# Optimization experiments

Measured on AMD Instinct MI355X. Metric: run time of the kernel, lower is better.

Reference implementation:

```python
import jax, jax.numpy as jnp
import numpy as np

B, OUT, IN = 1024, 1024, 512


def setup_inputs() -> dict:
    key = jax.random.key(0)
    kx, kw = jax.random.split(key)
    X = jax.random.normal(kx, (B, IN), dtype=jnp.float32)
    # Xavier-uniform init for W [out_features, in_features]
    limit = float(np.sqrt(6.0 / (IN + OUT)))
    W = jax.random.uniform(kw, (OUT, IN), dtype=jnp.float32, minval=-limit, maxval=limit)
    return {"X": X, "W": W}


def reference(X, W):
    # tropical min-plus + max-plus 'matmul':
    # out[b,o] = min_i(W[o,i] + X[b,i]) + max_i(W[o,i] + X[b,i])
    S = X[:, None, :] + W[None, :, :]  # [B, OUT, IN]
    return jnp.min(S, axis=-1) + jnp.max(S, axis=-1)  # [B, OUT]
```

## Files before the change

kernel.cpp:

```cpp
#include <hip/hip_runtime.h>
#include <math.h>


typedef float f4 __attribute__((ext_vector_type(4)));

constexpr int B_DIM  = 1024;
constexpr int O_DIM  = 1024;
constexpr int IN_DIM = 512;

constexpr int TM     = 64;
constexpr int TN     = 32;
constexpr int KW     = 128;
constexpr int BK     = 8;
constexpr int NSTAGE = KW / BK;

__global__ __launch_bounds__(256) void tropical_gemm(
    const float* __restrict__ X, const float* __restrict__ W,
    float* __restrict__ out) {
    __shared__ float lds[8192];

    const int tid  = threadIdx.x;
    const int w    = tid >> 6;
    const int lane = tid & 63;
    const int im   = lane >> 3;
    const int in_  = lane & 7;
    const int b0   = blockIdx.y * TM;
    const int o0   = blockIdx.x * TN;
    const int xoff = im * 8;
    const int woff = in_ * 4;
    const int wrow = lane >> 1;
    const int wk4  = (lane & 1) * 4;

    const float* Xp = X + (size_t)(b0 + lane) * IN_DIM + w * KW;
    const float* Wp = W + (size_t)(o0 + wrow) * IN_DIM + w * KW + wk4;

    float* wbase = &lds[w * 1536];

    float mn[8][4], mx[8][4];
#pragma unroll
    for (int i = 0; i < 8; ++i)
#pragma unroll
        for (int j = 0; j < 4; ++j) { mn[i][j] = INFINITY; mx[i][j] = -INFINITY; }

#define STAGE(bufsel)                                                         \
    do {                                                                      \
        float* d_ = wbase + (bufsel) * 768;                                   \
        _Pragma("unroll")                                                     \
        for (int j_ = 0; j_ < 4; ++j_) {                                      \
            d_[j_ * 64 + lane]       = xa[j_];                                \
            d_[(4 + j_) * 64 + lane] = xb[j_];                                \
            d_[512 + (wk4 + j_) * 32 + wrow] = wv[j_];                        \
        }                                                                     \
    } while (0)

#define LOADQ(P, kp)                                                          \
    do {                                                                      \
        P##x0  = *(const f4*)(sXf + (2 * (kp)) * 64 + xoff);                  \
        P##x0b = *(const f4*)(sXf + (2 * (kp)) * 64 + xoff + 4);              \
        P##x1  = *(const f4*)(sXf + (2 * (kp) + 1) * 64 + xoff);              \
        P##x1b = *(const f4*)(sXf + (2 * (kp) + 1) * 64 + xoff + 4);          \
        P##w0  = *(const f4*)(sWf + (2 * (kp)) * 32 + woff);                  \
        P##w1  = *(const f4*)(sWf + (2 * (kp) + 1) * 32 + woff);              \
    } while (0)

#define COMPUTE(P)                                                            \
    do {                                                                      \
        _Pragma("unroll")                                                     \
        for (int a_ = 0; a_ < 8; ++a_) {                                      \
            const float x0_ = (a_ < 4) ? P##x0[a_] : P##x0b[a_ - 4];          \
            const float x1_ = (a_ < 4) ? P##x1[a_] : P##x1b[a_ - 4];          \
            _Pragma("unroll")                                                 \
            for (int b_ = 0; b_ < 4; ++b_) {                                  \
                float s0_ = x0_ + P##w0[b_];                                  \
                float s1_ = x1_ + P##w1[b_];                                  \
                asm("v_min3_f32 %0, %1, %2, %0"                               \
                    : "+v"(mn[a_][b_]) : "v"(s0_), "v"(s1_));                 \
                asm("v_max3_f32 %0, %1, %2, %0"                               \
                    : "+v"(mx[a_][b_]) : "v"(s0_), "v"(s1_));                 \
            }                                                                 \
        }                                                                     \
    } while (0)

    f4 xa = *(const f4*)(Xp);
    f4 xb = *(const f4*)(Xp + 4);
    f4 wv = *(const f4*)(Wp);
    STAGE(0);

#pragma unroll 1
    for (int s = 0; s < NSTAGE; ++s) {
        if (s + 1 < NSTAGE) {
            xa = *(const f4*)(Xp + (s + 1) * BK);
            xb = *(const f4*)(Xp + (s + 1) * BK + 4);
            wv = *(const f4*)(Wp + (s + 1) * BK);
        }

        const float* sXf = wbase + (s & 1) * 768;
        const float* sWf = sXf + 512;

        f4 Ax0, Ax0b, Ax1, Ax1b, Aw0, Aw1;
        f4 Bx0, Bx0b, Bx1, Bx1b, Bw0, Bw1;

        LOADQ(A, 0);
        LOADQ(B, 1);
        COMPUTE(A);
        LOADQ(A, 2);
        COMPUTE(B);
        LOADQ(B, 3);
        COMPUTE(A);
        COMPUTE(B);

        if (s + 1 < NSTAGE) STAGE((s + 1) & 1);
    }
#undef STAGE
#undef LOADQ
#undef COMPUTE

#define DUMP_STATE(slotbase)                                                  \
    do {                                                                      \
        float* p_ = (slotbase) + lane * 4;                                    \
        _Pragma("unroll")                                                     \
        for (int r_ = 0; r_ < 8; ++r_) {                                      \
            *(float4*)(p_ + r_ * 256) =                                       \
                make_float4(mn[r_][0], mn[r_][1], mn[r_][2], mn[r_][3]);      \
            *(float4*)(p_ + (8 + r_) * 256) =                                 \
                make_float4(mx[r_][0], mx[r_][1], mx[r_][2], mx[r_][3]);      \
        }                                                                     \
    } while (0)

#define MERGE_STATE(slotbase)                                                 \
    do {                                                                      \
        const float* p_ = (slotbase) + lane * 4;                              \
        _Pragma("unroll")                                                     \
        for (int r_ = 0; r_ < 8; ++r_) {                                      \
            float4 vn_ = *(const float4*)(p_ + r_ * 256);                     \
            float4 vx_ = *(const float4*)(p_ + (8 + r_) * 256);               \
            mn[r_][0] = fminf(mn[r_][0], vn_.x);                              \
            mn[r_][1] = fminf(mn[r_][1], vn_.y);                              \
            mn[r_][2] = fminf(mn[r_][2], vn_.z);                              \
            mn[r_][3] = fminf(mn[r_][3], vn_.w);                              \
            mx[r_][0] = fmaxf(mx[r_][0], vx_.x);                              \
            mx[r_][1] = fmaxf(mx[r_][1], vx_.y);                              \
            mx[r_][2] = fmaxf(mx[r_][2], vx_.z);                              \
            mx[r_][3] = fmaxf(mx[r_][3], vx_.w);                              \
        }                                                                     \
    } while (0)

    float* slotA = lds;
    float* slotB = lds + 4096;

    __syncthreads();
    if (w == 2) DUMP_STATE(slotA);
    if (w == 3) DUMP_STATE(slotB);
    __syncthreads();
    if (w == 0) MERGE_STATE(slotA);
    if (w == 1) MERGE_STATE(slotB);
    __syncthreads();
    if (w == 1) DUMP_STATE(slotA);
    __syncthreads();
    if (w == 0) {
        MERGE_STATE(slotA);
        float* op = out + (size_t)(b0 + im * 8) * O_DIM + o0 + in_ * 4;
#pragma unroll
        for (int r = 0; r < 8; ++r)
            *(float4*)(op + (size_t)r * O_DIM) =
                make_float4(mn[r][0] + mx[r][0], mn[r][1] + mx[r][1],
                            mn[r][2] + mx[r][2], mn[r][3] + mx[r][3]);
    }
#undef DUMP_STATE
#undef MERGE_STATE
}

extern "C" void kernel_launch(void* const* d_in, const int* in_sizes, int n_in,
                              void* d_out, int out_size, void* d_ws, size_t ws_size,
                              hipStream_t stream) {
    (void)in_sizes; (void)n_in; (void)d_ws; (void)ws_size; (void)out_size;
    const float* X = (const float*)d_in[0];
    const float* W = (const float*)d_in[1];
    float* out     = (float*)d_out;

    dim3 grid(O_DIM / TN, B_DIM / TM);
    tropical_gemm<<<grid, dim3(256), 0, stream>>>(X, W, out);
}
```

Measured before the change: 31.66 us.

## Split K across eight waves per block with a deeper LDS reduction tree

Each block now runs 512 threads, and each of the eight waves handles a 64-wide K slice instead of four waves handling 128-wide slices. The per-wave pipeline gets half as many stages, and the final min/max merge becomes a three-level tree over four LDS slots. The software-pipelined A/B register double-buffering of LDS reads is replaced by a plain unrolled loop, leaving scheduling to the compiler. The aim is more parallel waves per tile to hide latency, at the cost of extra barriers and reduction traffic and doubled LDS per block.

Measured after the change: 33.74 us. 1.07x slower.

```diff
diff --git a/kernel.cpp b/kernel.cpp
--- a/kernel.cpp
+++ b/kernel.cpp
@@ -10,14 +10,14 @@
 
 constexpr int TM     = 64;
 constexpr int TN     = 32;
-constexpr int KW     = 128;
+constexpr int KW     = 64;
 constexpr int BK     = 8;
 constexpr int NSTAGE = KW / BK;
 
-__global__ __launch_bounds__(256) void tropical_gemm(
+__global__ __launch_bounds__(512, 4) void tropical_gemm(
     const float* __restrict__ X, const float* __restrict__ W,
     float* __restrict__ out) {
-    __shared__ float lds[8192];
+    __shared__ float lds[16384];
 
     const int tid  = threadIdx.x;
     const int w    = tid >> 6;
@@ -53,34 +53,6 @@
         }                                                                     \
     } while (0)
 
-#define LOADQ(P, kp)                                                          \
-    do {                                                                      \
-        P##x0  = *(const f4*)(sXf + (2 * (kp)) * 64 + xoff);                  \
-        P##x0b = *(const f4*)(sXf + (2 * (kp)) * 64 + xoff + 4);              \
-        P##x1  = *(const f4*)(sXf + (2 * (kp) + 1) * 64 + xoff);              \
-        P##x1b = *(const f4*)(sXf + (2 * (kp) + 1) * 64 + xoff + 4);          \
-        P##w0  = *(const f4*)(sWf + (2 * (kp)) * 32 + woff);                  \
-        P##w1  = *(const f4*)(sWf + (2 * (kp) + 1) * 32 + woff);              \
-    } while (0)
-
-#define COMPUTE(P)                                                            \
-    do {                                                                      \
-        _Pragma("unroll")                                                     \
-        for (int a_ = 0; a_ < 8; ++a_) {                                      \
-            const float x0_ = (a_ < 4) ? P##x0[a_] : P##x0b[a_ - 4];          \
-            const float x1_ = (a_ < 4) ? P##x1[a_] : P##x1b[a_ - 4];          \
-            _Pragma("unroll")                                                 \
-            for (int b_ = 0; b_ < 4; ++b_) {                                  \
-                float s0_ = x0_ + P##w0[b_];                                  \
-                float s1_ = x1_ + P##w1[b_];                                  \
-                asm("v_min3_f32 %0, %1, %2, %0"                               \
-                    : "+v"(mn[a_][b_]) : "v"(s0_), "v"(s1_));                 \
-                asm("v_max3_f32 %0, %1, %2, %0"                               \
-                    : "+v"(mx[a_][b_]) : "v"(s0_), "v"(s1_));                 \
-            }                                                                 \
-        }                                                                     \
-    } while (0)
-
     f4 xa = *(const f4*)(Xp);
     f4 xb = *(const f4*)(Xp + 4);
     f4 wv = *(const f4*)(Wp);
@@ -97,23 +69,33 @@
         const float* sXf = wbase + (s & 1) * 768;
         const float* sWf = sXf + 512;
 
-        f4 Ax0, Ax0b, Ax1, Ax1b, Aw0, Aw1;
-        f4 Bx0, Bx0b, Bx1, Bx1b, Bw0, Bw1;
-
-        LOADQ(A, 0);
-        LOADQ(B, 1);
-        COMPUTE(A);
-        LOADQ(A, 2);
-        COMPUTE(B);
-        LOADQ(B, 3);
-        COMPUTE(A);
-        COMPUTE(B);
+#pragma unroll
+        for (int kp = 0; kp < 4; ++kp) {
+            f4 x0  = *(const f4*)(sXf + (2 * kp) * 64 + xoff);
+            f4 x0b = *(const f4*)(sXf + (2 * kp) * 64 + xoff + 4);
+            f4 x1  = *(const f4*)(sXf + (2 * kp + 1) * 64 + xoff);
+            f4 x1b = *(const f4*)(sXf + (2 * kp + 1) * 64 + xoff + 4);
+            f4 w0  = *(const f4*)(sWf + (2 * kp) * 32 + woff);
+            f4 w1  = *(const f4*)(sWf + (2 * kp + 1) * 32 + woff);
+#pragma unroll
+            for (int a = 0; a < 8; ++a) {
+                const float xv0 = (a < 4) ? x0[a] : x0b[a - 4];
+                const float xv1 = (a < 4) ? x1[a] : x1b[a - 4];
+#pragma unroll
+                for (int b = 0; b < 4; ++b) {
+                    float s0 = xv0 + w0[b];
+                    float s1 = xv1 + w1[b];
+                    asm("v_min3_f32 %0, %1, %2, %0"
+                        : "+v"(mn[a][b]) : "v"(s0), "v"(s1));
+                    asm("v_max3_f32 %0, %1, %2, %0"
+                        : "+v"(mx[a][b]) : "v"(s0), "v"(s1));
+                }
+            }
+        }
 
         if (s + 1 < NSTAGE) STAGE((s + 1) & 1);
     }
 #undef STAGE
-#undef LOADQ
-#undef COMPUTE
 
 #define DUMP_STATE(slotbase)                                                  \
     do {                                                                      \
@@ -145,20 +127,32 @@
         }                                                                     \
     } while (0)
 
-    float* slotA = lds;
-    float* slotB = lds + 4096;
+    float* const slot0 = lds;
+    float* const slot1 = lds + 4096;
+    float* const slot2 = lds + 8192;
+    float* const slot3 = lds + 12288;
 
     __syncthreads();
-    if (w == 2) DUMP_STATE(slotA);
-    if (w == 3) DUMP_STATE(slotB);
+    if (w == 4) DUMP_STATE(slot0);
+    if (w == 5) DUMP_STATE(slot1);
+    if (w == 6) DUMP_STATE(slot2);
+    if (w == 7) DUMP_STATE(slot3);
     __syncthreads();
-    if (w == 0) MERGE_STATE(slotA);
-    if (w == 1) MERGE_STATE(slotB);
+    if (w == 0) MERGE_STATE(slot0);
+    if (w == 1) MERGE_STATE(slot1);
+    if (w == 2) MERGE_STATE(slot2);
+    if (w == 3) MERGE_STATE(slot3);
     __syncthreads();
-    if (w == 1) DUMP_STATE(slotA);
+    if (w == 2) DUMP_STATE(slot0);
+    if (w == 3) DUMP_STATE(slot1);
+    __syncthreads();
+    if (w == 0) MERGE_STATE(slot0);
+    if (w == 1) MERGE_STATE(slot1);
+    __syncthreads();
+    if (w == 1) DUMP_STATE(slot0);
     __syncthreads();
     if (w == 0) {
-        MERGE_STATE(slotA);
+        MERGE_STATE(slot0);
         float* op = out + (size_t)(b0 + im * 8) * O_DIM + o0 + in_ * 4;
 #pragma unroll
         for (int r = 0; r < 8; ++r)
@@ -179,5 +173,5 @@
     float* out     = (float*)d_out;
 
     dim3 grid(O_DIM / TN, B_DIM / TM);
-    tropical_gemm<<<grid, dim3(256), 0, stream>>>(X, W, out);
+    tropical_gemm<<<grid, dim3(512), 0, stream>>>(X, W, out);
 }
```

## Software-pipeline LDS reads and global prefetch across double-buffered stages

Applied to the files above, without the earlier changes.

Restructures the main loop to process two stages per iteration with four register fragment sets, so LDS reads for the next k-slice and the next stage are issued ahead of the min/max compute. Global prefetch now runs two stages ahead in two register sets. This is meant to hide LDS and global latency behind the v_min3/v_max3 compute. In exchange it uses more VGPRs, which may lower occupancy. It also relies on per-wave ordering of LDS writes and reads, since the wave writes a buffer it may still be reading from, with no barrier between.

Result: faster. 31.02 us (-2.0%).

```diff
diff --git a/kernel.cpp b/kernel.cpp
--- a/kernel.cpp
+++ b/kernel.cpp
@@ -42,25 +42,32 @@
 #pragma unroll
         for (int j = 0; j < 4; ++j) { mn[i][j] = INFINITY; mx[i][j] = -INFINITY; }
 
-#define STAGE(bufsel)                                                         \
+#define STAGE(bufsel, G)                                                      \
     do {                                                                      \
         float* d_ = wbase + (bufsel) * 768;                                   \
         _Pragma("unroll")                                                     \
         for (int j_ = 0; j_ < 4; ++j_) {                                      \
-            d_[j_ * 64 + lane]       = xa[j_];                                \
-            d_[(4 + j_) * 64 + lane] = xb[j_];                                \
-            d_[512 + (wk4 + j_) * 32 + wrow] = wv[j_];                        \
+            d_[j_ * 64 + lane]       = xa##G[j_];                             \
+            d_[(4 + j_) * 64 + lane] = xb##G[j_];                             \
+            d_[512 + (wk4 + j_) * 32 + wrow] = wv##G[j_];                     \
         }                                                                     \
     } while (0)
 
-#define LOADQ(P, kp)                                                          \
+#define PREFETCH(G, stg)                                                      \
     do {                                                                      \
-        P##x0  = *(const f4*)(sXf + (2 * (kp)) * 64 + xoff);                  \
-        P##x0b = *(const f4*)(sXf + (2 * (kp)) * 64 + xoff + 4);              \
-        P##x1  = *(const f4*)(sXf + (2 * (kp) + 1) * 64 + xoff);              \
-        P##x1b = *(const f4*)(sXf + (2 * (kp) + 1) * 64 + xoff + 4);          \
-        P##w0  = *(const f4*)(sWf + (2 * (kp)) * 32 + woff);                  \
-        P##w1  = *(const f4*)(sWf + (2 * (kp) + 1) * 32 + woff);              \
+        xa##G = *(const f4*)(Xp + (stg) * BK);                                \
+        xb##G = *(const f4*)(Xp + (stg) * BK + 4);                            \
+        wv##G = *(const f4*)(Wp + (stg) * BK);                                \
+    } while (0)
+
+#define LOADQ(P, cX, cW, kp)                                                  \
+    do {                                                                      \
+        P##x0  = *(const f4*)((cX) + (2 * (kp)) * 64 + xoff);                 \
+        P##x0b = *(const f4*)((cX) + (2 * (kp)) * 64 + xoff + 4);             \
+        P##x1  = *(const f4*)((cX) + (2 * (kp) + 1) * 64 + xoff);             \
+        P##x1b = *(const f4*)((cX) + (2 * (kp) + 1) * 64 + xoff + 4);         \
+        P##w0  = *(const f4*)((cW) + (2 * (kp)) * 32 + woff);                 \
+        P##w1  = *(const f4*)((cW) + (2 * (kp) + 1) * 32 + woff);             \
     } while (0)
 
 #define COMPUTE(P)                                                            \
@@ -81,37 +88,45 @@
         }                                                                     \
     } while (0)
 
-    f4 xa = *(const f4*)(Xp);
-    f4 xb = *(const f4*)(Xp + 4);
-    f4 wv = *(const f4*)(Wp);
-    STAGE(0);
+    f4 Ax0, Ax0b, Ax1, Ax1b, Aw0, Aw1;
+    f4 Bx0, Bx0b, Bx1, Bx1b, Bw0, Bw1;
+    f4 Cx0, Cx0b, Cx1, Cx1b, Cw0, Cw1;
+    f4 Dx0, Dx0b, Dx1, Dx1b, Dw0, Dw1;
+    f4 xa0, xb0, wv0, xa1, xb1, wv1;
+
+    const float* bX0 = wbase;
+    const float* bW0 = bX0 + 512;
+    const float* bX1 = wbase + 768;
+    const float* bW1 = bX1 + 512;
+
+    PREFETCH(0, 0);
+    STAGE(0, 0);
+    PREFETCH(1, 1);
+    LOADQ(A, bX0, bW0, 0);
+    LOADQ(B, bX0, bW0, 1);
 
 #pragma unroll 1
-    for (int s = 0; s < NSTAGE; ++s) {
-        if (s + 1 < NSTAGE) {
-            xa = *(const f4*)(Xp + (s + 1) * BK);
-            xb = *(const f4*)(Xp + (s + 1) * BK + 4);
-            wv = *(const f4*)(Wp + (s + 1) * BK);
+    for (int s2 = 0; s2 < 8; ++s2) {
+        LOADQ(C, bX0, bW0, 2);  COMPUTE(A);
+        LOADQ(D, bX0, bW0, 3);  COMPUTE(B);
+        STAGE(1, 1);
+        if (s2 < 7) PREFETCH(0, 2 * s2 + 2);
+        LOADQ(A, bX1, bW1, 0);  COMPUTE(C);
+        LOADQ(B, bX1, bW1, 1);  COMPUTE(D);
+
+        LOADQ(C, bX1, bW1, 2);  COMPUTE(A);
+        LOADQ(D, bX1, bW1, 3);  COMPUTE(B);
+        if (s2 < 7) {
+            STAGE(0, 0);
+            PREFETCH(1, 2 * s2 + 3);
+            LOADQ(A, bX0, bW0, 0);
         }
-
-        const float* sXf = wbase + (s & 1) * 768;
-        const float* sWf = sXf + 512;
-
-        f4 Ax0, Ax0b, Ax1, Ax1b, Aw0, Aw1;
-        f4 Bx0, Bx0b, Bx1, Bx1b, Bw0, Bw1;
-
-        LOADQ(A, 0);
-        LOADQ(B, 1);
-        COMPUTE(A);
-        LOADQ(A, 2);
-        COMPUTE(B);
-        LOADQ(B, 3);
-        COMPUTE(A);
-        COMPUTE(B);
-
-        if (s + 1 < NSTAGE) STAGE((s + 1) & 1);
+        COMPUTE(C);
+        if (s2 < 7) LOADQ(B, bX0, bW0, 1);
+        COMPUTE(D);
     }
 #undef STAGE
+#undef PREFETCH
 #undef LOADQ
 #undef COMPUTE
 
```

## Hand-schedule LDS pipeline with inline ds_read/write asm and packed f2 adds

Applied to the files above, without the earlier changes.

Replaces the compiler-scheduled LDS staging loop with hand-written ds_read_b128/ds_write_b64 inline asm, explicit lgkmcnt waits and sched barriers. Stages are software-pipelined across double buffers, and next-stage reads are issued before the current compute finishes. The LDS layout changes so each lane's 8 X rows are fetched with four b128 reads. Adds are done as 2-wide float vectors so they can map to packed FP32 adds. The goal is to hide LDS latency and cut VALU work. The cost is fragile manual waitcnt accounting and relying on wave-private buffers with no barriers.

Measured after the change: 34.30 us. +8.3%, slower.

```diff
diff --git a/kernel.cpp b/kernel.cpp
--- a/kernel.cpp
+++ b/kernel.cpp
@@ -1,18 +1,19 @@
 #include <hip/hip_runtime.h>
 #include <math.h>
+#include <stdint.h>
 
 
 typedef float f4 __attribute__((ext_vector_type(4)));
+typedef float f2 __attribute__((ext_vector_type(2)));
 
 constexpr int B_DIM  = 1024;
 constexpr int O_DIM  = 1024;
 constexpr int IN_DIM = 512;
 
-constexpr int TM     = 64;
-constexpr int TN     = 32;
-constexpr int KW     = 128;
-constexpr int BK     = 8;
-constexpr int NSTAGE = KW / BK;
+constexpr int TM = 64;
+constexpr int TN = 32;
+constexpr int KW = 128;
+constexpr int BK = 8;
 
 __global__ __launch_bounds__(256) void tropical_gemm(
     const float* __restrict__ X, const float* __restrict__ W,
@@ -26,15 +27,22 @@
     const int in_  = lane & 7;
     const int b0   = blockIdx.y * TM;
     const int o0   = blockIdx.x * TN;
-    const int xoff = im * 8;
-    const int woff = in_ * 4;
     const int wrow = lane >> 1;
     const int wk4  = (lane & 1) * 4;
 
     const float* Xp = X + (size_t)(b0 + lane) * IN_DIM + w * KW;
     const float* Wp = W + (size_t)(o0 + wrow) * IN_DIM + w * KW + wk4;
 
-    float* wbase = &lds[w * 1536];
+    const uint32_t lbase = (uint32_t)(uintptr_t)lds + w * 6144;
+    const uint32_t xr0 = lbase + im * 16;
+    const uint32_t xr1 = xr0 + 3072;
+    const uint32_t wr0 = lbase + 2048 + in_ * 32;
+    const uint32_t wr1 = wr0 + 3072;
+    const uint32_t xw0 = lbase + ((lane & 7) >> 1) * 128 + (lane & 1) * 8
+                               + (lane >> 3) * 16;
+    const uint32_t xw1 = xw0 + 3072;
+    const uint32_t ww0 = lbase + 2048 + wk4 * 128 + wrow * 8;
+    const uint32_t ww1 = ww0 + 3072;
 
     float mn[8][4], mx[8][4];
 #pragma unroll
@@ -42,78 +50,119 @@
 #pragma unroll
         for (int j = 0; j < 4; ++j) { mn[i][j] = INFINITY; mx[i][j] = -INFINITY; }
 
-#define STAGE(bufsel)                                                         \
-    do {                                                                      \
-        float* d_ = wbase + (bufsel) * 768;                                   \
-        _Pragma("unroll")                                                     \
-        for (int j_ = 0; j_ < 4; ++j_) {                                      \
-            d_[j_ * 64 + lane]       = xa[j_];                                \
-            d_[(4 + j_) * 64 + lane] = xb[j_];                                \
-            d_[512 + (wk4 + j_) * 32 + wrow] = wv[j_];                        \
-        }                                                                     \
-    } while (0)
-
-#define LOADQ(P, kp)                                                          \
-    do {                                                                      \
-        P##x0  = *(const f4*)(sXf + (2 * (kp)) * 64 + xoff);                  \
-        P##x0b = *(const f4*)(sXf + (2 * (kp)) * 64 + xoff + 4);              \
-        P##x1  = *(const f4*)(sXf + (2 * (kp) + 1) * 64 + xoff);              \
-        P##x1b = *(const f4*)(sXf + (2 * (kp) + 1) * 64 + xoff + 4);          \
-        P##w0  = *(const f4*)(sWf + (2 * (kp)) * 32 + woff);                  \
-        P##w1  = *(const f4*)(sWf + (2 * (kp) + 1) * 32 + woff);              \
+#define WAITL(N)                                                              \
+    do {                                                                      \
+        asm volatile("s_waitcnt lgkmcnt(%c0)" ::"i"(N) : "memory");           \
+        __builtin_amdgcn_sched_barrier(0);                                    \
+    } while (0)
+
+#define RD(P, XB, WB, KP)                                                     \
+    do {                                                                      \
+        asm volatile("ds_read_b128 %0, %1 offset:%c2"                         \
+                     : "=v"(P##x0) : "v"(XB), "i"((KP)*512 + 0));             \
+        asm volatile("ds_read_b128 %0, %1 offset:%c2"                         \
+                     : "=v"(P##x1) : "v"(XB), "i"((KP)*512 + 128));           \
+        asm volatile("ds_read_b128 %0, %1 offset:%c2"                         \
+                     : "=v"(P##x2) : "v"(XB), "i"((KP)*512 + 256));           \
+        asm volatile("ds_read_b128 %0, %1 offset:%c2"                         \
+                     : "=v"(P##x3) : "v"(XB), "i"((KP)*512 + 384));           \
+        asm volatile("ds_read_b128 %0, %1 offset:%c2"                         \
+                     : "=v"(P##w0) : "v"(WB), "i"((KP)*256 + 0));             \
+        asm volatile("ds_read_b128 %0, %1 offset:%c2"                         \
+                     : "=v"(P##w1) : "v"(WB), "i"((KP)*256 + 16));            \
+    } while (0)
+
+#define WRT(XB, WB)                                                           \
+    do {                                                                      \
+        f2 t0_ = __builtin_shufflevector(xa, xa, 0, 1);                       \
+        f2 t1_ = __builtin_shufflevector(xa, xa, 2, 3);                       \
+        f2 t2_ = __builtin_shufflevector(xb, xb, 0, 1);                       \
+        f2 t3_ = __builtin_shufflevector(xb, xb, 2, 3);                       \
+        f2 t4_ = __builtin_shufflevector(wv, wv, 0, 1);                       \
+        f2 t5_ = __builtin_shufflevector(wv, wv, 2, 3);                       \
+        asm volatile("ds_write_b64 %0, %1 offset:0"    ::"v"(XB), "v"(t0_) : "memory"); \
+        asm volatile("ds_write_b64 %0, %1 offset:512"  ::"v"(XB), "v"(t1_) : "memory"); \
+        asm volatile("ds_write_b64 %0, %1 offset:1024" ::"v"(XB), "v"(t2_) : "memory"); \
+        asm volatile("ds_write_b64 %0, %1 offset:1536" ::"v"(XB), "v"(t3_) : "memory"); \
+        asm volatile("ds_write_b64 %0, %1 offset:0"    ::"v"(WB), "v"(t4_) : "memory"); \
+        asm volatile("ds_write_b64 %0, %1 offset:256"  ::"v"(WB), "v"(t5_) : "memory"); \
+    } while (0)
+
+#define PF(STG)                                                               \
+    do {                                                                      \
+        xa = *(const f4*)(Xp + (STG) * BK);                                   \
+        xb = *(const f4*)(Xp + (STG) * BK + 4);                               \
+        wv = *(const f4*)(Wp + (STG) * BK);                                   \
+    } while (0)
+
+#define CW(XP, WQ, R, C0)                                                     \
+    do {                                                                      \
+        f2 wl_ = __builtin_shufflevector(WQ, WQ, 0, 1);                       \
+        f2 wh_ = __builtin_shufflevector(WQ, WQ, 2, 3);                       \
+        f2 s0_ = (XP) + wl_;                                                  \
+        f2 s1_ = (XP) + wh_;                                                  \
+        asm("v_min3_f32 %0, %1, %2, %0"                                       \
+            : "+v"(mn[R][C0]) : "v"(s0_[0]), "v"(s0_[1]));                    \
+        asm("v_max3_f32 %0, %1, %2, %0"                                       \
+            : "+v"(mx[R][C0]) : "v"(s0_[0]), "v"(s0_[1]));                    \
+        asm("v_min3_f32 %0, %1, %2, %0"                                       \
+            : "+v"(mn[R][(C0) + 1]) : "v"(s1_[0]), "v"(s1_[1]));              \
+        asm("v_max3_f32 %0, %1, %2, %0"                                       \
+            : "+v"(mx[R][(C0) + 1]) : "v"(s1_[0]), "v"(s1_[1]));              \
+    } while (0)
+
+#define CQ(P, XQ, R0)                                                         \
+    do {                                                                      \
+        f2 xl_ = __builtin_shufflevector(P##XQ, P##XQ, 0, 1);                 \
+        f2 xh_ = __builtin_shufflevector(P##XQ, P##XQ, 2, 3);                 \
+        CW(xl_, P##w0, (R0), 0);                                              \
+        CW(xh_, P##w0, (R0) + 1, 0);                                          \
+        CW(xl_, P##w1, (R0), 2);                                              \
+        CW(xh_, P##w1, (R0) + 1, 2);                                          \
     } while (0)
 
 #define COMPUTE(P)                                                            \
-    do {                                                                      \
-        _Pragma("unroll")                                                     \
-        for (int a_ = 0; a_ < 8; ++a_) {                                      \
-            const float x0_ = (a_ < 4) ? P##x0[a_] : P##x0b[a_ - 4];          \
-            const float x1_ = (a_ < 4) ? P##x1[a_] : P##x1b[a_ - 4];          \
-            _Pragma("unroll")                                                 \
-            for (int b_ = 0; b_ < 4; ++b_) {                                  \
-                float s0_ = x0_ + P##w0[b_];                                  \
-                float s1_ = x1_ + P##w1[b_];                                  \
-                asm("v_min3_f32 %0, %1, %2, %0"                               \
-                    : "+v"(mn[a_][b_]) : "v"(s0_), "v"(s1_));                 \
-                asm("v_max3_f32 %0, %1, %2, %0"                               \
-                    : "+v"(mx[a_][b_]) : "v"(s0_), "v"(s1_));                 \
-            }                                                                 \
-        }                                                                     \
-    } while (0)
-
-    f4 xa = *(const f4*)(Xp);
-    f4 xb = *(const f4*)(Xp + 4);
-    f4 wv = *(const f4*)(Wp);
-    STAGE(0);
+    do { CQ(P, x0, 0); CQ(P, x1, 2); CQ(P, x2, 4); CQ(P, x3, 6); } while (0)
+
+#define STAGE_BODY(XRC, WRC, XWN, WWN, XRN, WRN, PFS, DOPF, DOW, DONXT)       \
+    do {                                                                      \
+        WAITL(6);  COMPUTE(A); RD(A, XRC, WRC, 2);                 \
+        WAITL(6);  COMPUTE(B);                                     \
+        if (DOW) WRT(XWN, WWN);                                               \
+        if (DOPF) PF(PFS);                                                    \
+        RD(B, XRC, WRC, 3);                                                   \
+        WAITL((DOW) ? 12 : 6); COMPUTE(A);                         \
+        if (DONXT) RD(A, XRN, WRN, 0);                                        \
+        WAITL((DONXT) ? 6 : 0); COMPUTE(B);                        \
+        if (DONXT) RD(B, XRN, WRN, 1);                                        \
+    } while (0)
+
+    f4 Ax0, Ax1, Ax2, Ax3, Aw0, Aw1;
+    f4 Bx0, Bx1, Bx2, Bx3, Bw0, Bw1;
+    f4 xa, xb, wv;
+
+    PF(0);
+    WRT(xw0, ww0);
+    PF(1);
+    RD(A, xr0, wr0, 0);
+    RD(B, xr0, wr0, 1);
 
 #pragma unroll 1
-    for (int s = 0; s < NSTAGE; ++s) {
-        if (s + 1 < NSTAGE) {
-            xa = *(const f4*)(Xp + (s + 1) * BK);
-            xb = *(const f4*)(Xp + (s + 1) * BK + 4);
-            wv = *(const f4*)(Wp + (s + 1) * BK);
-        }
-
-        const float* sXf = wbase + (s & 1) * 768;
-        const float* sWf = sXf + 512;
-
-        f4 Ax0, Ax0b, Ax1, Ax1b, Aw0, Aw1;
-        f4 Bx0, Bx0b, Bx1, Bx1b, Bw0, Bw1;
-
-        LOADQ(A, 0);
-        LOADQ(B, 1);
-        COMPUTE(A);
-        LOADQ(A, 2);
-        COMPUTE(B);
-        LOADQ(B, 3);
-        COMPUTE(A);
-        COMPUTE(B);
-
-        if (s + 1 < NSTAGE) STAGE((s + 1) & 1);
+    for (int s2 = 0; s2 < 7; ++s2) {
+        STAGE_BODY(xr0, wr0, xw1, ww1, xr1, wr1, 2 * s2 + 2, 1, 1, 1);
+        STAGE_BODY(xr1, wr1, xw0, ww0, xr0, wr0, 2 * s2 + 3, 1, 1, 1);
     }
-#undef STAGE
-#undef LOADQ
+    STAGE_BODY(xr0, wr0, xw1, ww1, xr1, wr1, 0, 0, 1, 1);
+    STAGE_BODY(xr1, wr1, xw1, ww1, xr1, wr1, 0, 0, 0, 0);
+
+#undef WAITL
+#undef RD
+#undef WRT
+#undef PF
+#undef CW
+#undef CQ
 #undef COMPUTE
+#undef STAGE_BODY
 
 #define DUMP_STATE(slotbase)                                                  \
     do {                                                                      \
```
